# Performance work log

Hardware: AMD Instinct MI355X
Metric: run time of the kernel (lower is better)

The kernel has to match this reference:

```python
import jax, jax.numpy as jnp
import numpy as np

D = 512
F = 2048
H = 8
L = 128
B = 4


def _layer_norm(x, g, b, eps=1e-5):
    mu = jnp.mean(x, axis=-1, keepdims=True)
    var = jnp.var(x, axis=-1, keepdims=True)
    return (x - mu) * jax.lax.rsqrt(var + eps) * g + b


def _edge_mlp(Q, arc, W, b, arc_is_middle_out):
    # Equivalent to relu(Linear(concat(A, arc, B_))) with W: (3D, D), without
    # materializing the (B,L,L,3D) concat: split W into three D-blocks.
    # For W_out: concat(h_bf, arc, h_bf_t) -> block1 acts on Q[b,i], block3 on Q[b,j].
    # For W_in:  concat(h_bf_t, arc, h_bf) -> block1 acts on Q[b,j], block3 on Q[b,i].
    d = Q.shape[-1]
    W1, W2, W3 = W[:d], W[d:2 * d], W[2 * d:]
    mid = jnp.einsum('bijd,de->bije', arc, W2)
    if arc_is_middle_out:  # W_out ordering
        left = jnp.einsum('bid,de->bie', Q, W1)[:, :, None, :]   # broadcast over j
        right = jnp.einsum('bjd,de->bje', Q, W3)[:, None, :, :]  # broadcast over i
    else:  # W_in ordering
        left = jnp.einsum('bjd,de->bje', Q, W1)[:, None, :, :]
        right = jnp.einsum('bid,de->bie', Q, W3)[:, :, None, :]
    return jax.nn.relu(left + mid + right + b)


def _gat_attn(Q, KV, q_w, q_b, k_w, k_b, v_w, v_b, o_w, o_b):
    # Edge-conditioned multihead attention: per-query K/V of shape (B,L,L,D).
    bsz, seq, d = Q.shape
    dh = d // H
    scale = dh ** -0.5
    q = ((Q @ q_w + q_b) * scale).reshape(bsz, seq, H, dh)
    k = (KV @ k_w + k_b).reshape(bsz, seq, seq, H, dh)
    v = (KV @ v_w + v_b).reshape(bsz, seq, seq, H, dh)
    scores = jnp.einsum('bihd,bijhd->bhij', q, k)
    attn = jax.nn.softmax(scores, axis=-1)
    out = jnp.einsum('bhij,bijhd->bihd', attn, v).reshape(bsz, seq, d)
    return out @ o_w + o_b


def setup_inputs() -> dict:
    key = jax.random.key(0)
    ks = jax.random.split(key, 24)
    s = 0.02
    inp = {
        'h': jax.random.normal(ks[0], (L, B, D), jnp.float32),
        'src_outcoming_arc_x': jax.random.normal(ks[1], (B, L, L, D), jnp.float32),
        'src_incoming_arc_x': jax.random.normal(ks[2], (B, L, L, D), jnp.float32),
        'encoder_padding_mask': jnp.zeros((B, L), jnp.bool_),
        'W_out_w': jax.random.normal(ks[3], (3 * D, D), jnp.float32) * s,
        'W_out_b': jnp.zeros((D,), jnp.float32),
        'W_in_w': jax.random.normal(ks[4], (3 * D, D), jnp.float32) * s,
        'W_in_b': jnp.zeros((D,), jnp.float32),
        'q_w': jax.random.normal(ks[5], (D, D), jnp.float32) * s,
        'q_b': jnp.zeros((D,), jnp.float32),
        'k_w': jax.random.normal(ks[6], (D, D), jnp.float32) * s,
        'k_b': jnp.zeros((D,), jnp.float32),
        'v_w': jax.random.normal(ks[7], (D, D), jnp.float32) * s,
        'v_b': jnp.zeros((D,), jnp.float32),
        'o_w': jax.random.normal(ks[8], (D, D), jnp.float32) * s,
        'o_b': jnp.zeros((D,), jnp.float32),
        'ln1_g': jnp.ones((D,), jnp.float32),
        'ln1_b': jnp.zeros((D,), jnp.float32),
        'fc1_w': jax.random.normal(ks[9], (D, F), jnp.float32) * s,
        'fc1_b': jnp.zeros((F,), jnp.float32),
        'fc2_w': jax.random.normal(ks[10], (F, D), jnp.float32) * s,
        'fc2_b': jnp.zeros((D,), jnp.float32),
        'ln2_g': jnp.ones((D,), jnp.float32),
        'ln2_b': jnp.zeros((D,), jnp.float32),
    }
    return inp


def reference(h, src_outcoming_arc_x, src_incoming_arc_x, encoder_padding_mask,
              W_out_w, W_out_b, W_in_w, W_in_b,
              q_w, q_b, k_w, k_b, v_w, v_b, o_w, o_b,
              ln1_g, ln1_b, fc1_w, fc1_b, fc2_w, fc2_b, ln2_g, ln2_b):
    # h: (L, B, D). Dropouts are identity (eval). attn_mask=None.
    residual = h
    Q = jnp.transpose(h, (1, 0, 2))  # (B, L, D)
    U_out = _edge_mlp(Q, src_outcoming_arc_x, W_out_w, W_out_b, True)
    att_out = _gat_attn(Q, U_out, q_w, q_b, k_w, k_b, v_w, v_b, o_w, o_b)
    U_in = _edge_mlp(Q, src_incoming_arc_x, W_in_w, W_in_b, False)
    att_in = _gat_attn(Q, U_in, q_w, q_b, k_w, k_b, v_w, v_b, o_w, o_b)
    x = jnp.transpose(att_in + att_out, (1, 0, 2))  # back to (L, B, D)
    x = _layer_norm(residual + x, ln1_g, ln1_b)
    residual = x
    x = jax.nn.relu(x @ fc1_w + fc1_b) @ fc2_w + fc2_b
    x = _layer_norm(residual + x, ln2_g, ln2_b)
    return x
```

## Files before the change

kernel.cpp:

```cpp
#include <hip/hip_runtime.h>
#include <stdint.h>
#include <stddef.h>

#define NTOK 512
#define NM   65536

typedef __bf16 bf16x8 __attribute__((ext_vector_type(8)));
typedef float  f32x4  __attribute__((ext_vector_type(4)));
typedef unsigned int u32x4 __attribute__((ext_vector_type(4)));

__device__ __forceinline__ unsigned short f2bf(float f) {
    unsigned int u = __builtin_bit_cast(unsigned int, f);
    u += 0x7FFFu + ((u >> 16) & 1u);
    return (unsigned short)(u >> 16);
}
__device__ __forceinline__ float bf2f(unsigned short s) {
    unsigned int u = ((unsigned int)s) << 16;
    return __builtin_bit_cast(float, u);
}

__device__ __forceinline__ void gload16(const void* g, void* l) {
    __builtin_amdgcn_global_load_lds(
        (const __attribute__((address_space(1))) void*)g,
        (__attribute__((address_space(3))) void*)l,
        16, 0, 0);
}

__global__ __launch_bounds__(256) void k_qtrans(const float* __restrict__ h,
                                                unsigned short* __restrict__ Qm) {
    int idx = blockIdx.x * 256 + threadIdx.x;
    int tok = idx >> 9, d = idx & 511;
    int b = tok >> 7, i = tok & 127;
    Qm[idx] = f2bf(h[(i * 4 + b) * 512 + d]);
}

struct TRJob { const float* src; unsigned short* dst; int srcLd, dstLd, tcols; float scale; };
struct TRJobs { TRJob j[11]; int start[12]; };

__global__ __launch_bounds__(256) void k_trN(TRJobs js) {
    __shared__ float tile[64][65];
    int b = blockIdx.x;
    int ji = 0;
    while (ji < 10 && b >= js.start[ji + 1]) ++ji;
    TRJob jb = js.j[ji];
    int rel = b - js.start[ji];
    int bx = rel % jb.tcols, by = rel / jb.tcols;
    int r0 = by * 64, c0 = bx * 64;
    int t = threadIdx.x;
    int c = t & 63, rr = t >> 6;
    #pragma unroll
    for (int ii = 0; ii < 16; ++ii) {
        int r = ii * 4 + rr;
        tile[r][c] = jb.src[(size_t)(r0 + r) * jb.srcLd + c0 + c];
    }
    __syncthreads();
    #pragma unroll
    for (int ii = 0; ii < 16; ++ii) {
        int n = ii * 4 + rr;
        jb.dst[(size_t)(c0 + n) * jb.dstLd + r0 + c] = f2bf(tile[c][n] * jb.scale);
    }
}

__global__ __launch_bounds__(256) void k_kwT(const float* __restrict__ kw,
                                             float* __restrict__ kwT) {
    int idx = blockIdx.x * 256 + threadIdx.x;
    kwT[idx] = kw[(size_t)(idx & 511) * 512 + (idx >> 9)];
}
__global__ __launch_bounds__(256) void k_bias1(const float* __restrict__ Wob,
                                               const float* __restrict__ Wib,
                                               const float* __restrict__ qb,
                                               float* __restrict__ bias1) {
    int i = blockIdx.x * 256 + threadIdx.x;
    if (i >= 2560) return;
    float v = 0.f;
    if (i < 512) v = Wob[i];
    else if (i < 1024) v = 0.f;
    else if (i < 1536) v = Wib[i - 1024];
    else if (i < 2048) v = 0.f;
    else v = qb[i - 2048] * 0.125f;
    bias1[i] = v;
}

struct MMP {
    const unsigned short* A;  int lda;
    const unsigned short* Bt; int ldb;
    const float* bias;
    const float* accs;
    float* outF;
    unsigned short* outB;
    int ldo;
    int K;
    int relu;
    int aOffPerN64;
    int zKOff;
    int zOutOff;
};

__global__ __launch_bounds__(256) void k_mm(MMP p) {
    __shared__ unsigned char As[64 * 128];
    __shared__ unsigned char Bs[64 * 128];
    int t = threadIdx.x;
    int lane = t & 63, w = t >> 6;
    int m0 = blockIdx.x * 64, n0 = blockIdx.y * 64;
    int z = blockIdx.z;
    const unsigned short* A  = p.A + (size_t)(n0 >> 6) * p.aOffPerN64 + (size_t)z * p.zKOff;
    const unsigned short* Bt = p.Bt + (size_t)z * p.zKOff;
    int wm = (w >> 1) * 32, wn = (w & 1) * 32;
    f32x4 acc[2][2];
    #pragma unroll
    for (int a = 0; a < 2; ++a)
        #pragma unroll
        for (int b = 0; b < 2; ++b) acc[a][b] = (f32x4){0.f, 0.f, 0.f, 0.f};

    for (int kb = 0; kb < p.K; kb += 64) {
        __syncthreads();
        #pragma unroll
        for (int s = 0; s < 2; ++s) {
            int c = t + s * 256;
            int r = c >> 3, kc = (c & 7) * 8;
            int off = (r * 128 + kc * 2) ^ ((r & 7) << 4);
            *reinterpret_cast<u32x4*>(As + off) =
                *reinterpret_cast<const u32x4*>(A + (size_t)(m0 + r) * p.lda + kb + kc);
            *reinterpret_cast<u32x4*>(Bs + off) =
                *reinterpret_cast<const u32x4*>(Bt + (size_t)(n0 + r) * p.ldb + kb + kc);
        }
        __syncthreads();
        #pragma unroll
        for (int kh = 0; kh < 2; ++kh) {
            int kk = kh * 32 + (lane >> 4) * 8;
            bf16x8 af[2], bfr[2];
            #pragma unroll
            for (int mf = 0; mf < 2; ++mf) {
                int r = wm + mf * 16 + (lane & 15);
                int off = (r * 128 + kk * 2) ^ ((r & 7) << 4);
                af[mf] = *reinterpret_cast<const bf16x8*>(As + off);
            }
            #pragma unroll
            for (int nf = 0; nf < 2; ++nf) {
                int r = wn + nf * 16 + (lane & 15);
                int off = (r * 128 + kk * 2) ^ ((r & 7) << 4);
                bfr[nf] = *reinterpret_cast<const bf16x8*>(Bs + off);
            }
            #pragma unroll
            for (int mf = 0; mf < 2; ++mf)
                #pragma unroll
                for (int nf = 0; nf < 2; ++nf)
                    acc[mf][nf] = __builtin_amdgcn_mfma_f32_16x16x32_bf16(
                        af[mf], bfr[nf], acc[mf][nf], 0, 0, 0);
        }
    }
    #pragma unroll
    for (int mf = 0; mf < 2; ++mf) {
        #pragma unroll
        for (int rr = 0; rr < 4; ++rr) {
            int gm = m0 + wm + mf * 16 + (lane >> 4) * 4 + rr;
            #pragma unroll
            for (int nf = 0; nf < 2; ++nf) {
                int e = n0 + wn + nf * 16 + (lane & 15);
                float v = acc[mf][nf][rr];
                if (p.bias) v += p.bias[e];
                if (p.relu) v = fmaxf(v, 0.f);
                if (p.accs) v += p.accs[(size_t)gm * p.ldo + e];
                size_t oo = (size_t)gm * p.ldo + e + (size_t)z * p.zOutOff;
                if (p.outF) p.outF[oo] = v;
                if (p.outB) p.outB[oo] = f2bf(v);
            }
        }
    }
}

__global__ __launch_bounds__(256) void k_prep2(const float* __restrict__ qs, int qld,
                                               const float* __restrict__ kwT,
                                               const float* __restrict__ k_b,
                                               unsigned short* __restrict__ p,
                                               float* __restrict__ c) {
    __shared__ float q8[8][512];
    int t = threadIdx.x;
    int tok0 = blockIdx.x * 8;
    int d = blockIdx.y * 256 + t;
    for (int idx = t; idx < 4096; idx += 256) {
        int s = idx >> 9, dd = idx & 511;
        q8[s][dd] = qs[(size_t)(tok0 + s) * qld + dd];
    }
    __syncthreads();
    if (blockIdx.y == 0 && t < 64) {
        int s = t >> 3, hh = t & 7;
        float cv = 0.f;
        for (int dh = 0; dh < 64; ++dh) cv += k_b[hh * 64 + dh] * q8[s][hh * 64 + dh];
        c[(tok0 + s) * 8 + hh] = cv;
    }
    for (int hh = 0; hh < 8; ++hh) {
        float pv[8];
        #pragma unroll
        for (int s = 0; s < 8; ++s) pv[s] = 0.f;
        for (int dh = 0; dh < 64; ++dh) {
            float wv = kwT[(size_t)(hh * 64 + dh) * 512 + d];
            #pragma unroll
            for (int s = 0; s < 8; ++s) pv[s] += wv * q8[s][hh * 64 + dh];
        }
        #pragma unroll
        for (int s = 0; s < 8; ++s)
            p[((size_t)(tok0 + s) * 8 + hh) * 512 + d] = f2bf(pv[s]);
    }
}

__global__ __launch_bounds__(256) void k_midU(const float* __restrict__ arc,
                                              const unsigned short* __restrict__ W2t,
                                              const float* __restrict__ fixedMat, int fld,
                                              const float* __restrict__ rowMat, int rld,
                                              unsigned short* __restrict__ U) {
    __shared__ float As4[128 * 64];
    __shared__ unsigned short Bs2[128 * 64];
    int t = threadIdx.x;
    int lane = t & 63;
    int w = t >> 6;
    int bid = blockIdx.x;
    int xcd = bid & 7, slot = bid >> 3;
    int mt = xcd * 64 + (slot >> 2);
    int nt = slot & 3;
    int m0 = mt * 128;
    int n0 = nt * 128;
    int wm = (w >> 1) * 64, wn = (w & 1) * 64;
    f32x4 acc[4][4];
    #pragma unroll
    for (int a = 0; a < 4; ++a)
        #pragma unroll
        for (int bq = 0; bq < 4; ++bq) acc[a][bq] = (f32x4){0.f, 0.f, 0.f, 0.f};

    int arA = lane >> 4;
    int acb = lane & 15;
    int brB = lane >> 3;
    int bcb = lane & 7;

    for (int kb8 = 0; kb8 < 8; ++kb8) {
        int kb = kb8 * 64;
        __syncthreads();
        #pragma unroll
        for (int i = 0; i < 8; ++i) {
            int base = (w * 8 + i) * 1024;
            int r = ((w * 8 + i) << 2) + arA;
            int cs = acb ^ (r & 7);
            gload16(arc + (size_t)(m0 + r) * 512 + kb + cs * 4,
                    (char*)As4 + base);
        }
        #pragma unroll
        for (int i = 0; i < 4; ++i) {
            int base = (w * 4 + i) * 1024;
            int r = ((w * 4 + i) << 3) + brB;
            int cs = bcb ^ (r & 7);
            gload16(W2t + (size_t)(n0 + r) * 512 + kb + cs * 8,
                    (char*)Bs2 + base);
        }
        __syncthreads();
        #pragma unroll
        for (int kh = 0; kh < 2; ++kh) {
            int kk = kh * 32 + (lane >> 4) * 8;
            bf16x8 af[4], bfr[4];
            #pragma unroll
            for (int mf = 0; mf < 4; ++mf) {
                int rr = wm + mf * 16 + (lane & 15);
                int c0 = kk >> 2;
                const char* bp = (const char*)As4 + rr * 256;
                float4 a0 = *reinterpret_cast<const float4*>(bp + ((c0 ^ (rr & 7)) << 4));
                float4 a1 = *reinterpret_cast<const float4*>(bp + (((c0 + 1) ^ (rr & 7)) << 4));
                af[mf][0] = (__bf16)a0.x; af[mf][1] = (__bf16)a0.y;
                af[mf][2] = (__bf16)a0.z; af[mf][3] = (__bf16)a0.w;
                af[mf][4] = (__bf16)a1.x; af[mf][5] = (__bf16)a1.y;
                af[mf][6] = (__bf16)a1.z; af[mf][7] = (__bf16)a1.w;
            }
            #pragma unroll
            for (int nf = 0; nf < 4; ++nf) {
                int rn = wn + nf * 16 + (lane & 15);
                int c = kk >> 3;
                bfr[nf] = *reinterpret_cast<const bf16x8*>(
                    (const char*)Bs2 + rn * 128 + ((c ^ (rn & 7)) << 4));
            }
            #pragma unroll
            for (int mf = 0; mf < 4; ++mf)
                #pragma unroll
                for (int nf = 0; nf < 4; ++nf)
                    acc[mf][nf] = __builtin_amdgcn_mfma_f32_16x16x32_bf16(
                        af[mf], bfr[nf], acc[mf][nf], 0, 0, 0);
        }
    }
    int tokI = mt;
    int bb = mt >> 7;
    float fx[4];
    #pragma unroll
    for (int nf = 0; nf < 4; ++nf)
        fx[nf] = fixedMat[(size_t)tokI * fld + n0 + wn + nf * 16 + (lane & 15)];
    #pragma unroll
    for (int mf = 0; mf < 4; ++mf) {
        #pragma unroll
        for (int r = 0; r < 4; ++r) {
            int row = wm + mf * 16 + (lane >> 4) * 4 + r;
            int gm = m0 + row;
            int tokJ = bb * 128 + (gm & 127);
            const float* rv = rowMat + (size_t)tokJ * rld;
            #pragma unroll
            for (int nf = 0; nf < 4; ++nf) {
                int e = n0 + wn + nf * 16 + (lane & 15);
                float v = acc[mf][nf][r] + fx[nf] + rv[e];
                v = fmaxf(v, 0.f);
                U[(size_t)gm * 512 + e] = f2bf(v);
            }
        }
    }
}

__global__ __launch_bounds__(256) void k_scores(const unsigned short* __restrict__ U,
                                                const unsigned short* __restrict__ p,
                                                const float* __restrict__ c,
                                                float* __restrict__ attn) {
    __shared__ float sc[8][128];
    int tok = blockIdx.x;
    int t = threadIdx.x;
    int w = t >> 6;
    int lane = t & 63;
    int hh = lane & 15;
    int kg = lane >> 4;
    bool hv = hh < 8;
    f32x4 acc[2];
    acc[0] = (f32x4){0.f, 0.f, 0.f, 0.f};
    acc[1] = (f32x4){0.f, 0.f, 0.f, 0.f};
    const unsigned short* Ub = U + (size_t)tok * 65536 + (size_t)(w * 32) * 512;
    const unsigned short* pb = p + ((size_t)tok * 8 + (hh & 7)) * 512;
    for (int ks = 0; ks < 16; ++ks) {
        int kcol = ks * 32 + kg * 8;
        u32x4 braw = (u32x4){0u, 0u, 0u, 0u};
        if (hv) braw = *reinterpret_cast<const u32x4*>(pb + kcol);
        bf16x8 bfrag = __builtin_bit_cast(bf16x8, braw);
        #pragma unroll
        for (int mf = 0; mf < 2; ++mf) {
            bf16x8 afrag = *reinterpret_cast<const bf16x8*>(
                Ub + (size_t)(mf * 16 + hh) * 512 + kcol);
            acc[mf] = __builtin_amdgcn_mfma_f32_16x16x32_bf16(afrag, bfrag, acc[mf], 0, 0, 0);
        }
    }
    if (hv) {
        float cval = c[tok * 8 + hh];
        #pragma unroll
        for (int mf = 0; mf < 2; ++mf)
            #pragma unroll
            for (int r = 0; r < 4; ++r)
                sc[hh][w * 32 + mf * 16 + kg * 4 + r] = acc[mf][r] + cval;
    }
    __syncthreads();
    int h2 = t >> 5, l32 = t & 31;
    float v0 = sc[h2][l32], v1 = sc[h2][l32 + 32],
          v2 = sc[h2][l32 + 64], v3 = sc[h2][l32 + 96];
    float mx = fmaxf(fmaxf(v0, v1), fmaxf(v2, v3));
    #pragma unroll
    for (int o = 16; o >= 1; o >>= 1) mx = fmaxf(mx, __shfl_xor(mx, o));
    float e0 = __expf(v0 - mx), e1 = __expf(v1 - mx),
          e2 = __expf(v2 - mx), e3 = __expf(v3 - mx);
    float sum = e0 + e1 + e2 + e3;
    #pragma unroll
    for (int o = 16; o >= 1; o >>= 1) sum += __shfl_xor(sum, o);
    float inv = 1.f / sum;
    float* ab = attn + (size_t)tok * 1024 + h2 * 128;
    ab[l32]      = e0 * inv;
    ab[l32 + 32] = e1 * inv;
    ab[l32 + 64] = e2 * inv;
    ab[l32 + 96] = e3 * inv;
}

__global__ __launch_bounds__(256) void k_wacc(const unsigned short* __restrict__ U,
                                              const float* __restrict__ attn,
                                              unsigned short* __restrict__ Wacc) {
    __shared__ float at[1024];
    int t = threadIdx.x;
    int tok = blockIdx.x;
    for (int idx = t; idx < 1024; idx += 256) at[idx] = attn[(size_t)tok * 1024 + idx];
    __syncthreads();
    int d0 = t * 2;
    const unsigned short* Ub = U + (size_t)tok * 65536;
    float acc[8][2];
    #pragma unroll
    for (int hh = 0; hh < 8; ++hh) { acc[hh][0] = 0.f; acc[hh][1] = 0.f; }
    for (int j = 0; j < 128; ++j) {
        unsigned int uv = *reinterpret_cast<const unsigned int*>(Ub + (size_t)j * 512 + d0);
        float u0 = bf2f((unsigned short)(uv & 0xffffu));
        float u1 = bf2f((unsigned short)(uv >> 16));
        #pragma unroll
        for (int hh = 0; hh < 8; ++hh) {
            float a = at[hh * 128 + j];
            acc[hh][0] += a * u0;
            acc[hh][1] += a * u1;
        }
    }
    #pragma unroll
    for (int hh = 0; hh < 8; ++hh) {
        unsigned short* wp = Wacc + ((size_t)tok * 8 + hh) * 512 + d0;
        wp[0] = f2bf(acc[hh][0]);
        wp[1] = f2bf(acc[hh][1]);
    }
}

__global__ __launch_bounds__(256) void k_ln(const float* __restrict__ A,
                                            const float* __restrict__ Bv, int bswap,
                                            const float* __restrict__ parts,
                                            const float* __restrict__ pbias,
                                            const float* __restrict__ g,
                                            const float* __restrict__ bta,
                                            float* __restrict__ outF,
                                            unsigned short* __restrict__ outB) {
    int t = threadIdx.x;
    int tok = blockIdx.x;
    size_t aoff = (size_t)tok * 512;
    float b0, b1;
    if (parts) {
        b0 = parts[aoff + t] + parts[262144 + aoff + t] +
             parts[524288 + aoff + t] + parts[786432 + aoff + t] + pbias[t];
        b1 = parts[aoff + t + 256] + parts[262144 + aoff + t + 256] +
             parts[524288 + aoff + t + 256] + parts[786432 + aoff + t + 256] + pbias[t + 256];
    } else {
        size_t boff = aoff;
        if (bswap) { int i = tok >> 2, b = tok & 3; boff = (size_t)(b * 128 + i) * 512; }
        b0 = Bv[boff + t];
        b1 = Bv[boff + t + 256];
    }
    float v0 = A[aoff + t] + b0;
    float v1 = A[aoff + t + 256] + b1;
    float s = v0 + v1, q = v0 * v0 + v1 * v1;
    #pragma unroll
    for (int o = 32; o >= 1; o >>= 1) { s += __shfl_xor(s, o); q += __shfl_xor(q, o); }
    __shared__ float red[8];
    int w = t >> 6, lane = t & 63;
    if (lane == 0) { red[w] = s; red[4 + w] = q; }
    __syncthreads();
    float ts = red[0] + red[1] + red[2] + red[3];
    float tq = red[4] + red[5] + red[6] + red[7];
    float mean = ts * (1.f / 512.f);
    float var = tq * (1.f / 512.f) - mean * mean;
    float inv = rsqrtf(var + 1e-5f);
    float o0 = (v0 - mean) * inv * g[t] + bta[t];
    float o1 = (v1 - mean) * inv * g[t + 256] + bta[t + 256];
    outF[aoff + t] = o0;
    outF[aoff + t + 256] = o1;
    if (outB) { outB[aoff + t] = f2bf(o0); outB[aoff + t + 256] = f2bf(o1); }
}

extern "C" void kernel_launch(void* const* d_in, const int* in_sizes, int n_in,
                              void* d_out, int out_size, void* d_ws, size_t ws_size,
                              hipStream_t stream) {
    (void)in_sizes; (void)n_in; (void)out_size; (void)ws_size;
    const float* h       = (const float*)d_in[0];
    const float* arc_out = (const float*)d_in[1];
    const float* arc_in  = (const float*)d_in[2];
    const float* W_out_w = (const float*)d_in[4];
    const float* W_out_b = (const float*)d_in[5];
    const float* W_in_w  = (const float*)d_in[6];
    const float* W_in_b  = (const float*)d_in[7];
    const float* q_w  = (const float*)d_in[8];
    const float* q_b  = (const float*)d_in[9];
    const float* k_w  = (const float*)d_in[10];
    const float* k_b  = (const float*)d_in[11];
    const float* v_w  = (const float*)d_in[12];
    const float* v_b  = (const float*)d_in[13];
    const float* o_w  = (const float*)d_in[14];
    const float* o_b  = (const float*)d_in[15];
    const float* ln1_g = (const float*)d_in[16];
    const float* ln1_b = (const float*)d_in[17];
    const float* fc1_w = (const float*)d_in[18];
    const float* fc1_b = (const float*)d_in[19];
    const float* fc2_w = (const float*)d_in[20];
    const float* fc2_b = (const float*)d_in[21];
    const float* ln2_g = (const float*)d_in[22];
    const float* ln2_b = (const float*)d_in[23];
    float* out = (float*)d_out;

    char* wsb = (char*)d_ws;
    size_t off = 0;
    auto ALLOC = [&](size_t bytes) -> void* {
        void* ptr = wsb + off;
        off += (bytes + 255) & ~(size_t)255;
        return ptr;
    };
    unsigned short* WcatT = (unsigned short*)ALLOC((size_t)2560 * 512 * 2);
    unsigned short* W2to  = (unsigned short*)ALLOC(262144 * 2);
    unsigned short* W2ti  = (unsigned short*)ALLOC(262144 * 2);
    unsigned short* o_wT  = (unsigned short*)ALLOC(262144 * 2);
    unsigned short* v_wT  = (unsigned short*)ALLOC(262144 * 2);
    unsigned short* fc1T  = (unsigned short*)ALLOC((size_t)2048 * 512 * 2);
    unsigned short* fc2T  = (unsigned short*)ALLOC((size_t)512 * 2048 * 2);
    float* kwT   = (float*)ALLOC(262144 * 4);
    float* bias1 = (float*)ALLOC(2560 * 4);
    unsigned short* Qm = (unsigned short*)ALLOC(262144 * 2);
    float* QWcat = (float*)ALLOC((size_t)512 * 2560 * 4);
    unsigned short* pbuf = (unsigned short*)ALLOC((size_t)NTOK * 8 * 512 * 2);
    float* cbuf = (float*)ALLOC(NTOK * 8 * 4);
    unsigned short* Ubuf = (unsigned short*)ALLOC((size_t)NM * 512 * 2);
    float* attnb = (float*)ALLOC((size_t)NTOK * 8 * 128 * 4);
    unsigned short* Waccb = (unsigned short*)ALLOC((size_t)NTOK * 8 * 512 * 2);
    unsigned short* tmpb  = (unsigned short*)ALLOC(262144 * 2);
    float* attsum = (float*)ALLOC(262144 * 4);
    float* x1  = (float*)ALLOC(262144 * 4);
    unsigned short* x1b = (unsigned short*)ALLOC(262144 * 2);
    unsigned short* ybb = (unsigned short*)ALLOC((size_t)NTOK * 2048 * 2);
    float* zparts = (float*)ALLOC((size_t)4 * 262144 * 4);

    k_qtrans<<<1024, 256, 0, stream>>>(h, Qm);

    {
        TRJobs js = {};
        auto SET = [&](int i, const float* s, int sld, unsigned short* d, int dld,
                       float sc, int tiles, int tcols) {
            js.j[i] = TRJob{s, d, sld, dld, tcols, sc};
            js.start[i + 1] = js.start[i] + tiles;
        };
        js.start[0] = 0;
        SET(0,  W_out_w,              512, WcatT,              512, 1.f,    64, 8);
        SET(1,  W_out_w + 1024 * 512, 512, WcatT + 512 * 512,  512, 1.f,    64, 8);
        SET(2,  W_in_w,               512, WcatT + 1024 * 512, 512, 1.f,    64, 8);
        SET(3,  W_in_w + 1024 * 512,  512, WcatT + 1536 * 512, 512, 1.f,    64, 8);
        SET(4,  q_w,                  512, WcatT + 2048 * 512, 512, 0.125f, 64, 8);
        SET(5,  W_out_w + 512 * 512,  512, W2to,               512, 1.f,    64, 8);
        SET(6,  W_in_w + 512 * 512,   512, W2ti,               512, 1.f,    64, 8);
        SET(7,  o_w,                  512, o_wT,               512, 1.f,    64, 8);
        SET(8,  v_w,                  512, v_wT,               512, 1.f,    64, 8);
        SET(9,  fc1_w,               2048, fc1T,               512, 1.f,   256, 32);
        SET(10, fc2_w,                512, fc2T,              2048, 1.f,   256, 8);
        k_trN<<<js.start[11], 256, 0, stream>>>(js);
    }
    k_kwT<<<1024, 256, 0, stream>>>(k_w, kwT);
    k_bias1<<<10, 256, 0, stream>>>(W_out_b, W_in_b, q_b, bias1);

    {
        MMP m = {};
        m.A = Qm; m.lda = 512; m.Bt = WcatT; m.ldb = 512;
        m.bias = bias1; m.outF = QWcat; m.ldo = 2560; m.K = 512;
        k_mm<<<dim3(8, 40), 256, 0, stream>>>(m);
    }
    k_prep2<<<dim3(64, 2), 256, 0, stream>>>(QWcat + 2048, 2560, kwT, k_b, pbuf, cbuf);

    for (int arc = 0; arc < 2; ++arc) {
        const float* arcp = (arc == 0) ? arc_out : arc_in;
        const unsigned short* w2 = (arc == 0) ? W2to : W2ti;
        const float* fixedM = (arc == 0) ? QWcat + 0    : QWcat + 1536;
        const float* rowM   = (arc == 0) ? QWcat + 512  : QWcat + 1024;
        k_midU<<<2048, 256, 0, stream>>>(arcp, w2, fixedM, 2560, rowM, 2560, Ubuf);
        k_scores<<<512, 256, 0, stream>>>(Ubuf, pbuf, cbuf, attnb);
        k_wacc<<<512, 256, 0, stream>>>(Ubuf, attnb, Waccb);
        {
            MMP m = {};
            m.A = Waccb; m.lda = 4096; m.aOffPerN64 = 512;
            m.Bt = v_wT; m.ldb = 512;
            m.bias = v_b; m.outB = tmpb; m.ldo = 512; m.K = 512;
            k_mm<<<dim3(8, 8), 256, 0, stream>>>(m);
        }
        {
            MMP m = {};
            m.A = tmpb; m.lda = 512; m.Bt = o_wT; m.ldb = 512;
            m.bias = o_b; m.outF = attsum; m.ldo = 512; m.K = 512;
            m.accs = (arc == 0) ? nullptr : attsum;
            k_mm<<<dim3(8, 8), 256, 0, stream>>>(m);
        }
    }

    k_ln<<<512, 256, 0, stream>>>(h, attsum, 1, nullptr, nullptr, ln1_g, ln1_b, x1, x1b);

    {
        MMP m = {};
        m.A = x1b; m.lda = 512; m.Bt = fc1T; m.ldb = 512;
        m.bias = fc1_b; m.relu = 1; m.outB = ybb; m.ldo = 2048; m.K = 512;
        k_mm<<<dim3(8, 32), 256, 0, stream>>>(m);
    }
    {
        MMP m = {};
        m.A = ybb; m.lda = 2048; m.Bt = fc2T; m.ldb = 2048;
        m.outF = zparts; m.ldo = 512; m.K = 512;
        m.zKOff = 512; m.zOutOff = 262144;
        k_mm<<<dim3(8, 8, 4), 256, 0, stream>>>(m);
    }
    k_ln<<<512, 256, 0, stream>>>(x1, nullptr, 0, zparts, fc2_b, ln2_g, ln2_b, out, nullptr);
}
```

Measured before the change: 372.8 us.

## Fuse scores+softmax+weighted sum and merge both arcs before V/O projections

Fuses the score, softmax and attention-weighted U accumulation kernels into one, which keeps the attention weights in shared memory instead of writing them to global. Uses linearity to sum the two arcs' weighted-U results first, so the V and O projection GEMMs run once with doubled biases instead of twice. Also merges three small prep kernels into one launch. The cost is an extra fp32 Wsum buffer that must be written and read back between arcs.

```diff
diff --git a/kernel.cpp b/kernel.cpp
--- a/kernel.cpp
+++ b/kernel.cpp
@@ -26,12 +26,36 @@
         16, 0, 0);
 }
 
-__global__ __launch_bounds__(256) void k_qtrans(const float* __restrict__ h,
-                                                unsigned short* __restrict__ Qm) {
-    int idx = blockIdx.x * 256 + threadIdx.x;
-    int tok = idx >> 9, d = idx & 511;
-    int b = tok >> 7, i = tok & 127;
-    Qm[idx] = f2bf(h[(i * 4 + b) * 512 + d]);
+__global__ __launch_bounds__(256) void k_prep(const float* __restrict__ h,
+                                              unsigned short* __restrict__ Qm,
+                                              const float* __restrict__ kw,
+                                              float* __restrict__ kwT,
+                                              const float* __restrict__ Wob,
+                                              const float* __restrict__ Wib,
+                                              const float* __restrict__ qb,
+                                              float* __restrict__ bias1) {
+    int bid = blockIdx.x;
+    int t = threadIdx.x;
+    if (bid < 1024) {
+        int idx = bid * 256 + t;
+        int tok = idx >> 9, d = idx & 511;
+        int b = tok >> 7, i = tok & 127;
+        Qm[idx] = f2bf(h[(i * 4 + b) * 512 + d]);
+    } else if (bid < 2048) {
+        int idx = (bid - 1024) * 256 + t;
+        kwT[idx] = kw[(size_t)(idx & 511) * 512 + (idx >> 9)];
+    } else {
+        int i = (bid - 2048) * 256 + t;
+        if (i < 2560) {
+            float v = 0.f;
+            if (i < 512) v = Wob[i];
+            else if (i < 1024) v = 0.f;
+            else if (i < 1536) v = Wib[i - 1024];
+            else if (i < 2048) v = 0.f;
+            else v = qb[i - 2048] * 0.125f;
+            bias1[i] = v;
+        }
+    }
 }
 
 struct TRJob { const float* src; unsigned short* dst; int srcLd, dstLd, tcols; float scale; };
@@ -59,26 +83,6 @@
         int n = ii * 4 + rr;
         jb.dst[(size_t)(c0 + n) * jb.dstLd + r0 + c] = f2bf(tile[c][n] * jb.scale);
     }
-}
-
-__global__ __launch_bounds__(256) void k_kwT(const float* __restrict__ kw,
-                                             float* __restrict__ kwT) {
-    int idx = blockIdx.x * 256 + threadIdx.x;
-    kwT[idx] = kw[(size_t)(idx & 511) * 512 + (idx >> 9)];
-}
-__global__ __launch_bounds__(256) void k_bias1(const float* __restrict__ Wob,
-                                               const float* __restrict__ Wib,
-                                               const float* __restrict__ qb,
-                                               float* __restrict__ bias1) {
-    int i = blockIdx.x * 256 + threadIdx.x;
-    if (i >= 2560) return;
-    float v = 0.f;
-    if (i < 512) v = Wob[i];
-    else if (i < 1024) v = 0.f;
-    else if (i < 1536) v = Wib[i - 1024];
-    else if (i < 2048) v = 0.f;
-    else v = qb[i - 2048] * 0.125f;
-    bias1[i] = v;
 }
 
 struct MMP {
@@ -94,6 +98,7 @@
     int aOffPerN64;
     int zKOff;
     int zOutOff;
+    float biasScale;
 };
 
 __global__ __launch_bounds__(256) void k_mm(MMP p) {
@@ -158,7 +163,7 @@
             for (int nf = 0; nf < 2; ++nf) {
                 int e = n0 + wn + nf * 16 + (lane & 15);
                 float v = acc[mf][nf][rr];
-                if (p.bias) v += p.bias[e];
+                if (p.bias) v += p.bias[e] * p.biasScale;
                 if (p.relu) v = fmaxf(v, 0.f);
                 if (p.accs) v += p.accs[(size_t)gm * p.ldo + e];
                 size_t oo = (size_t)gm * p.ldo + e + (size_t)z * p.zOutOff;
@@ -308,11 +313,13 @@
     }
 }
 
-__global__ __launch_bounds__(256) void k_scores(const unsigned short* __restrict__ U,
-                                                const unsigned short* __restrict__ p,
-                                                const float* __restrict__ c,
-                                                float* __restrict__ attn) {
-    __shared__ float sc[8][128];
+__global__ __launch_bounds__(256) void k_att2(const unsigned short* __restrict__ U,
+                                              const unsigned short* __restrict__ p,
+                                              const float* __restrict__ c,
+                                              float* __restrict__ Wsum,
+                                              unsigned short* __restrict__ Waccb,
+                                              int accum) {
+    __shared__ float at[8][128];
     int tok = blockIdx.x;
     int t = threadIdx.x;
     int w = t >> 6;
@@ -323,7 +330,8 @@
     f32x4 acc[2];
     acc[0] = (f32x4){0.f, 0.f, 0.f, 0.f};
     acc[1] = (f32x4){0.f, 0.f, 0.f, 0.f};
-    const unsigned short* Ub = U + (size_t)tok * 65536 + (size_t)(w * 32) * 512;
+    const unsigned short* Ub0 = U + (size_t)tok * 65536;
+    const unsigned short* Ub = Ub0 + (size_t)(w * 32) * 512;
     const unsigned short* pb = p + ((size_t)tok * 8 + (hh & 7)) * 512;
     for (int ks = 0; ks < 16; ++ks) {
         int kcol = ks * 32 + kg * 8;
@@ -343,57 +351,55 @@
         for (int mf = 0; mf < 2; ++mf)
             #pragma unroll
             for (int r = 0; r < 4; ++r)
-                sc[hh][w * 32 + mf * 16 + kg * 4 + r] = acc[mf][r] + cval;
+                at[hh][w * 32 + mf * 16 + kg * 4 + r] = acc[mf][r] + cval;
     }
     __syncthreads();
-    int h2 = t >> 5, l32 = t & 31;
-    float v0 = sc[h2][l32], v1 = sc[h2][l32 + 32],
-          v2 = sc[h2][l32 + 64], v3 = sc[h2][l32 + 96];
-    float mx = fmaxf(fmaxf(v0, v1), fmaxf(v2, v3));
-    #pragma unroll
-    for (int o = 16; o >= 1; o >>= 1) mx = fmaxf(mx, __shfl_xor(mx, o));
-    float e0 = __expf(v0 - mx), e1 = __expf(v1 - mx),
-          e2 = __expf(v2 - mx), e3 = __expf(v3 - mx);
-    float sum = e0 + e1 + e2 + e3;
-    #pragma unroll
-    for (int o = 16; o >= 1; o >>= 1) sum += __shfl_xor(sum, o);
-    float inv = 1.f / sum;
-    float* ab = attn + (size_t)tok * 1024 + h2 * 128;
-    ab[l32]      = e0 * inv;
-    ab[l32 + 32] = e1 * inv;
-    ab[l32 + 64] = e2 * inv;
-    ab[l32 + 96] = e3 * inv;
-}
-
-__global__ __launch_bounds__(256) void k_wacc(const unsigned short* __restrict__ U,
-                                              const float* __restrict__ attn,
-                                              unsigned short* __restrict__ Wacc) {
-    __shared__ float at[1024];
-    int t = threadIdx.x;
-    int tok = blockIdx.x;
-    for (int idx = t; idx < 1024; idx += 256) at[idx] = attn[(size_t)tok * 1024 + idx];
+    {
+        int h2 = t >> 5, l32 = t & 31;
+        float v0 = at[h2][l32], v1 = at[h2][l32 + 32],
+              v2 = at[h2][l32 + 64], v3 = at[h2][l32 + 96];
+        float mx = fmaxf(fmaxf(v0, v1), fmaxf(v2, v3));
+        #pragma unroll
+        for (int o = 16; o >= 1; o >>= 1) mx = fmaxf(mx, __shfl_xor(mx, o));
+        float e0 = __expf(v0 - mx), e1 = __expf(v1 - mx),
+              e2 = __expf(v2 - mx), e3 = __expf(v3 - mx);
+        float sum = e0 + e1 + e2 + e3;
+        #pragma unroll
+        for (int o = 16; o >= 1; o >>= 1) sum += __shfl_xor(sum, o);
+        float inv = 1.f / sum;
+        at[h2][l32]      = e0 * inv;
+        at[h2][l32 + 32] = e1 * inv;
+        at[h2][l32 + 64] = e2 * inv;
+        at[h2][l32 + 96] = e3 * inv;
+    }
     __syncthreads();
     int d0 = t * 2;
-    const unsigned short* Ub = U + (size_t)tok * 65536;
-    float acc[8][2];
-    #pragma unroll
-    for (int hh = 0; hh < 8; ++hh) { acc[hh][0] = 0.f; acc[hh][1] = 0.f; }
+    float a8[8][2];
+    #pragma unroll
+    for (int q = 0; q < 8; ++q) { a8[q][0] = 0.f; a8[q][1] = 0.f; }
     for (int j = 0; j < 128; ++j) {
-        unsigned int uv = *reinterpret_cast<const unsigned int*>(Ub + (size_t)j * 512 + d0);
+        unsigned int uv = *reinterpret_cast<const unsigned int*>(Ub0 + (size_t)j * 512 + d0);
         float u0 = bf2f((unsigned short)(uv & 0xffffu));
         float u1 = bf2f((unsigned short)(uv >> 16));
         #pragma unroll
-        for (int hh = 0; hh < 8; ++hh) {
-            float a = at[hh * 128 + j];
-            acc[hh][0] += a * u0;
-            acc[hh][1] += a * u1;
-        }
-    }
-    #pragma unroll
-    for (int hh = 0; hh < 8; ++hh) {
-        unsigned short* wp = Wacc + ((size_t)tok * 8 + hh) * 512 + d0;
-        wp[0] = f2bf(acc[hh][0]);
-        wp[1] = f2bf(acc[hh][1]);
+        for (int q = 0; q < 8; ++q) {
+            float a = at[q][j];
+            a8[q][0] += a * u0;
+            a8[q][1] += a * u1;
+        }
+    }
+    #pragma unroll
+    for (int q = 0; q < 8; ++q) {
+        size_t woff = ((size_t)tok * 8 + q) * 512 + d0;
+        if (!accum) {
+            Wsum[woff] = a8[q][0];
+            Wsum[woff + 1] = a8[q][1];
+        } else {
+            float s0 = Wsum[woff] + a8[q][0];
+            float s1 = Wsum[woff + 1] + a8[q][1];
+            Waccb[woff] = f2bf(s0);
+            Waccb[woff + 1] = f2bf(s1);
+        }
     }
 }
 
@@ -491,7 +497,7 @@
     unsigned short* pbuf = (unsigned short*)ALLOC((size_t)NTOK * 8 * 512 * 2);
     float* cbuf = (float*)ALLOC(NTOK * 8 * 4);
     unsigned short* Ubuf = (unsigned short*)ALLOC((size_t)NM * 512 * 2);
-    float* attnb = (float*)ALLOC((size_t)NTOK * 8 * 128 * 4);
+    float* Wsum = (float*)ALLOC((size_t)NTOK * 8 * 512 * 4);
     unsigned short* Waccb = (unsigned short*)ALLOC((size_t)NTOK * 8 * 512 * 2);
     unsigned short* tmpb  = (unsigned short*)ALLOC(262144 * 2);
     float* attsum = (float*)ALLOC(262144 * 4);
@@ -500,7 +506,7 @@
     unsigned short* ybb = (unsigned short*)ALLOC((size_t)NTOK * 2048 * 2);
     float* zparts = (float*)ALLOC((size_t)4 * 262144 * 4);
 
-    k_qtrans<<<1024, 256, 0, stream>>>(h, Qm);
+    k_prep<<<2058, 256, 0, stream>>>(h, Qm, k_w, kwT, W_out_b, W_in_b, q_b, bias1);
 
     {
         TRJobs js = {};
@@ -523,13 +529,12 @@
         SET(10, fc2_w,                512, fc2T,              2048, 1.f,   256, 8);
         k_trN<<<js.start[11], 256, 0, stream>>>(js);
     }
-    k_kwT<<<1024, 256, 0, stream>>>(k_w, kwT);
-    k_bias1<<<10, 256, 0, stream>>>(W_out_b, W_in_b, q_b, bias1);
 
     {
         MMP m = {};
         m.A = Qm; m.lda = 512; m.Bt = WcatT; m.ldb = 512;
-        m.bias = bias1; m.outF = QWcat; m.ldo = 2560; m.K = 512;
+        m.bias = bias1; m.biasScale = 1.f;
+        m.outF = QWcat; m.ldo = 2560; m.K = 512;
         k_mm<<<dim3(8, 40), 256, 0, stream>>>(m);
     }
     k_prep2<<<dim3(64, 2), 256, 0, stream>>>(QWcat + 2048, 2560, kwT, k_b, pbuf, cbuf);
@@ -540,22 +545,23 @@
         const float* fixedM = (arc == 0) ? QWcat + 0    : QWcat + 1536;
         const float* rowM   = (arc == 0) ? QWcat + 512  : QWcat + 1024;
         k_midU<<<2048, 256, 0, stream>>>(arcp, w2, fixedM, 2560, rowM, 2560, Ubuf);
-        k_scores<<<512, 256, 0, stream>>>(Ubuf, pbuf, cbuf, attnb);
-        k_wacc<<<512, 256, 0, stream>>>(Ubuf, attnb, Waccb);
-        {
-            MMP m = {};
-            m.A = Waccb; m.lda = 4096; m.aOffPerN64 = 512;
-            m.Bt = v_wT; m.ldb = 512;
-            m.bias = v_b; m.outB = tmpb; m.ldo = 512; m.K = 512;
-            k_mm<<<dim3(8, 8), 256, 0, stream>>>(m);
-        }
-        {
-            MMP m = {};
-            m.A = tmpb; m.lda = 512; m.Bt = o_wT; m.ldb = 512;
-            m.bias = o_b; m.outF = attsum; m.ldo = 512; m.K = 512;
-            m.accs = (arc == 0) ? nullptr : attsum;
-            k_mm<<<dim3(8, 8), 256, 0, stream>>>(m);
-        }
+        k_att2<<<512, 256, 0, stream>>>(Ubuf, pbuf, cbuf, Wsum, Waccb, arc);
+    }
+
+    {
+        MMP m = {};
+        m.A = Waccb; m.lda = 4096; m.aOffPerN64 = 512;
+        m.Bt = v_wT; m.ldb = 512;
+        m.bias = v_b; m.biasScale = 2.f;
+        m.outB = tmpb; m.ldo = 512; m.K = 512;
+        k_mm<<<dim3(8, 8), 256, 0, stream>>>(m);
+    }
+    {
+        MMP m = {};
+        m.A = tmpb; m.lda = 512; m.Bt = o_wT; m.ldb = 512;
+        m.bias = o_b; m.biasScale = 2.f;
+        m.outF = attsum; m.ldo = 512; m.K = 512;
+        k_mm<<<dim3(8, 8), 256, 0, stream>>>(m);
     }
 
     k_ln<<<512, 256, 0, stream>>>(h, attsum, 1, nullptr, nullptr, ln1_g, ln1_b, x1, x1b);
@@ -563,7 +569,8 @@
     {
         MMP m = {};
         m.A = x1b; m.lda = 512; m.Bt = fc1T; m.ldb = 512;
-        m.bias = fc1_b; m.relu = 1; m.outB = ybb; m.ldo = 2048; m.K = 512;
+        m.bias = fc1_b; m.biasScale = 1.f;
+        m.relu = 1; m.outB = ybb; m.ldo = 2048; m.K = 512;
         k_mm<<<dim3(8, 32), 256, 0, stream>>>(m);
     }
     {
```

New measurement: 342.3 us. 8.2% less time.
